# Kernel tuning notes

Hardware: AMD Instinct MI355X
Metric: run time of the kernel (lower is better)

The kernel has to match this reference:

```python
import jax, jax.numpy as jnp
import numpy as np

_SAMPLING_EPS = 1e-5
B, V = 256, 128000


def _apply_min_p(logits, min_p):
    # probs >= min_p * max_prob  <=>  keep; else logit -> -inf
    probs = jax.nn.softmax(logits, axis=-1)
    max_probs = jnp.max(probs, axis=-1, keepdims=True)
    keep = probs >= (min_p[:, None] * max_probs)
    return jnp.where(keep, logits, -jnp.inf)


def _apply_top_k_top_p(logits, top_k, top_p):
    # Sort ascending once; derive per-row keep-thresholds for both filters.
    logits_sort = jnp.sort(logits, axis=-1)  # [B, V] ascending
    # top-k threshold: value at position V-k (kth largest)
    k_idx = jnp.clip(V - top_k, 0, V - 1).astype(jnp.int32)
    k_thresh = jnp.take_along_axis(logits_sort, k_idx[:, None], axis=-1)  # [B,1]
    # top-p: on ascending-sorted probs, token is kept iff cumsum > 1 - p
    probs_sort = jax.nn.softmax(logits_sort, axis=-1)
    probs_cum = jnp.cumsum(probs_sort, axis=-1)
    kept = probs_cum > (1.0 - top_p[:, None])
    kept = kept.at[:, -1].set(True)  # always keep the max-prob token
    p_thresh = jnp.min(jnp.where(kept, logits_sort, jnp.inf), axis=-1, keepdims=True)
    thresh = jnp.maximum(k_thresh, p_thresh)
    return jnp.where(logits >= thresh, logits, -jnp.inf)


def setup_inputs() -> dict:
    key = jax.random.key(0)
    k1, k2, k3, k4, k5 = jax.random.split(key, 5)
    logits = jax.random.normal(k1, (B, V), jnp.float32)
    temperature = jax.random.uniform(k2, (B,), jnp.float32, 0.1, 1.5)
    temperature = temperature.at[:8].set(0.0)  # greedy rows
    min_p = jax.random.uniform(k3, (B,), jnp.float32, 0.0, 0.2)
    top_k = jax.random.randint(k4, (B,), 1, 64).astype(jnp.int32)
    top_p = jax.random.uniform(k5, (B,), jnp.float32, 0.5, 1.0)
    return {"logits": logits, "temperature": temperature, "min_p": min_p,
            "top_k": top_k, "top_p": top_p}


def reference(logits, temperature, min_p, top_k, top_p):
    logits = logits.astype(jnp.float32)
    greedy = jnp.argmax(logits, axis=-1)  # [B]
    # safe temperature divide (greedy rows have temp ~ 0 but are overridden)
    safe_t = jnp.where(temperature < _SAMPLING_EPS, 1.0, temperature)
    scaled = logits / safe_t[:, None]
    scaled = _apply_min_p(scaled, min_p)
    masked = _apply_top_k_top_p(scaled, top_k, top_p)
    # Gumbel-max trick == categorical sampling from softmax(masked)
    u = jax.random.uniform(jax.random.key(42), masked.shape, jnp.float32, 1e-10, 1.0)
    gumbel = -jnp.log(-jnp.log(u))
    random_sampled = jnp.argmax(masked + gumbel, axis=-1)
    sampled = jnp.where(temperature < _SAMPLING_EPS, greedy, random_sampled)
    return sampled[:, None]  # sampled_token_ids [B, 1]
```

## Files before the change

### kernel.cpp

```cpp
#include <hip/hip_runtime.h>
#include <stdint.h>

typedef unsigned long long u64;
typedef unsigned int u32;

#define VOCAB 128000
#define NV4   32000
#define NROWS 256
#define BLK   1024
#define NW    16
#define NB    4096
#define CAPL  4096
#define SEPS  1e-5f
#define LN2X40 27.725887222397812f

__device__ __forceinline__ u32 f2key(float f){
  u32 u = __float_as_uint(f);
  return (u & 0x80000000u) ? ~u : (u | 0x80000000u);
}
__device__ __forceinline__ float key2f(u32 k){
  u32 u = (k & 0x80000000u) ? (k ^ 0x80000000u) : ~k;
  return __uint_as_float(u);
}

__device__ __forceinline__ void tf2x32(u32 x0, u32 x1, u32 &o0, u32 &o1){
  const u32 k0 = 0u, k1 = 42u, k2 = 0u ^ 42u ^ 0x1BD11BDAu;
  x0 += k0; x1 += k1;
#define TFR(r) { x0 += x1; x1 = (x1 << (r)) | (x1 >> (32 - (r))); x1 ^= x0; }
  TFR(13) TFR(15) TFR(26) TFR(6)
  x0 += k1; x1 += k2 + 1u;
  TFR(17) TFR(29) TFR(16) TFR(24)
  x0 += k2; x1 += k0 + 2u;
  TFR(13) TFR(15) TFR(26) TFR(6)
  x0 += k0; x1 += k1 + 3u;
  TFR(17) TFR(29) TFR(16) TFR(24)
  x0 += k1; x1 += k2 + 4u;
  TFR(13) TFR(15) TFR(26) TFR(6)
  x0 += k2; x1 += k0 + 5u;
#undef TFR
  o0 = x0; o1 = x1;
}
__device__ __forceinline__ u32 gumbel_bits(u32 i){
  u32 o0, o1; tf2x32(0u, i, o0, o1);
  return o0 ^ o1;
}
__device__ __forceinline__ float bits2gumbel(u32 b){
  float f = __uint_as_float(0x3F800000u | (b >> 9)) - 1.0f;
  float u = fmaxf(1e-10f, f + 1e-10f);
  return -logf(-logf(u));
}

__device__ __forceinline__ void cross4096_u32(
    const u32* arr, u32* aux, u32 target, u32* out_idx, u32* out_before, int t)
{
  aux[t] = arr[4*t+0] + arr[4*t+1] + arr[4*t+2] + arr[4*t+3];
  __syncthreads();
  if (t < 64){
    u32 gs = 0u;
    #pragma unroll
    for (int j=0;j<16;j++) gs += aux[t*16+j];
    u32 pref = gs;
    #pragma unroll
    for (int d=1; d<64; d<<=1){ u32 v = __shfl_up(pref, d, 64); if (t >= d) pref += v; }
    u64 bal = __ballot(pref > target);
    int g = bal ? (__ffsll((long long)bal) - 1) : 63;
    u32 pg = __shfl(pref, g, 64);
    u32 gg = __shfl(gs, g, 64);
    if (t == 0){
      u32 c = pg - gg;
      u32 idx = (u32)(g*64 + 63);
      for (int j=0;j<16;j++){
        u32 v = aux[g*16+j];
        if (c + v > target){
          int base = (g*16+j)*4;
          for (int q=0;q<4;q++){
            u32 w = arr[base+q];
            if (c + w > target){ idx = (u32)(base+q); goto doneu; }
            c += w;
          }
        }
        c += v;
      }
      doneu:
      *out_idx = idx; *out_before = c;
    }
  }
}

__device__ __forceinline__ void cross4096_u64(
    const u64* arr, u64* aux, u64 target, u32* out_idx, u64* out_before, int t)
{
  aux[t] = arr[4*t+0] + arr[4*t+1] + arr[4*t+2] + arr[4*t+3];
  __syncthreads();
  if (t < 64){
    u64 gs = 0ull;
    #pragma unroll
    for (int j=0;j<16;j++) gs += aux[t*16+j];
    u64 pref = gs;
    #pragma unroll
    for (int d=1; d<64; d<<=1){
      u64 v = __shfl_up((unsigned long long)pref, d, 64); if (t >= d) pref += v;
    }
    u64 bal = __ballot(pref > target);
    int g = bal ? (__ffsll((long long)bal) - 1) : 63;
    u64 pg = __shfl((unsigned long long)pref, g, 64);
    u64 gg = __shfl((unsigned long long)gs, g, 64);
    if (t == 0){
      u64 c = pg - gg;
      u32 idx = (u32)(g*64 + 63);
      for (int j=0;j<16;j++){
        u64 v = aux[g*16+j];
        if (c + v > target){
          int base = (g*16+j)*4;
          for (int q=0;q<4;q++){
            u64 w = arr[base+q];
            if (c + w > target){ idx = (u32)(base+q); goto donev; }
            c += w;
          }
        }
        c += v;
      }
      donev:
      *out_idx = idx; *out_before = c;
    }
  }
}

__device__ __forceinline__ void cross4096_mass(
    const u64* arr, u64* aux, float topp_v, u64* out_target,
    u32* out_idx, u64* out_before, int t)
{
  aux[t] = arr[4*t+0] + arr[4*t+1] + arr[4*t+2] + arr[4*t+3];
  __syncthreads();
  if (t < 64){
    u64 gs = 0ull;
    #pragma unroll
    for (int j=0;j<16;j++) gs += aux[t*16+j];
    u64 pref = gs;
    #pragma unroll
    for (int d=1; d<64; d<<=1){
      u64 v = __shfl_up((unsigned long long)pref, d, 64); if (t >= d) pref += v;
    }
    u64 total = __shfl((unsigned long long)pref, 63, 64);
    u64 target = (u64)((double)(1.0f - topp_v) * (double)total);
    u64 bal = __ballot(pref > target);
    int g = bal ? (__ffsll((long long)bal) - 1) : 63;
    u64 pg = __shfl((unsigned long long)pref, g, 64);
    u64 gg = __shfl((unsigned long long)gs, g, 64);
    if (t == 0){
      u64 c = pg - gg;
      u32 idx = (u32)(g*64 + 63);
      for (int j=0;j<16;j++){
        u64 v = aux[g*16+j];
        if (c + v > target){
          int base = (g*16+j)*4;
          for (int q=0;q<4;q++){
            u64 w = arr[base+q];
            if (c + w > target){ idx = (u32)(base+q); goto donem; }
            c += w;
          }
        }
        c += v;
      }
      donem:
      *out_target = target; *out_idx = idx; *out_before = c;
    }
  }
}

__device__ __forceinline__ void cross256_u32(const u32* arr, u32 target, u32* out_idx, int t){
  if (t < 64){
    u32 gs = arr[4*t+0]+arr[4*t+1]+arr[4*t+2]+arr[4*t+3];
    u32 pref = gs;
    #pragma unroll
    for (int d=1; d<64; d<<=1){ u32 v=__shfl_up(pref,d,64); if (t>=d) pref+=v; }
    u64 bal = __ballot(pref > target);
    int g = bal ? (__ffsll((long long)bal)-1) : 63;
    u32 pg=__shfl(pref,g,64), gg=__shfl(gs,g,64);
    if (t==0){
      u32 c = pg-gg; u32 idx=(u32)(g*4+3);
      for (int q=0;q<4;q++){ u32 w=arr[g*4+q]; if (c+w>target){ idx=(u32)(g*4+q); break; } c+=w; }
      *out_idx = idx;
    }
  }
}
__device__ __forceinline__ void cross256_u64(const u64* arr, u64 target, u32* out_idx, int t){
  if (t < 64){
    u64 gs = arr[4*t+0]+arr[4*t+1]+arr[4*t+2]+arr[4*t+3];
    u64 pref = gs;
    #pragma unroll
    for (int d=1; d<64; d<<=1){
      u64 v=__shfl_up((unsigned long long)pref,d,64); if (t>=d) pref+=v;
    }
    u64 bal = __ballot(pref > target);
    int g = bal ? (__ffsll((long long)bal)-1) : 63;
    u64 pg=__shfl((unsigned long long)pref,g,64), gg=__shfl((unsigned long long)gs,g,64);
    if (t==0){
      u64 c = pg-gg; u32 idx=(u32)(g*4+3);
      for (int q=0;q<4;q++){ u64 w=arr[g*4+q]; if (c+w>target){ idx=(u32)(g*4+q); break; } c+=w; }
      *out_idx = idx;
    }
  }
}

__device__ __forceinline__ void msmerge(float &m1, float &S1, float m2, float S2){
  float mm = fmaxf(m1, m2);
  if (mm == -INFINITY){ m1 = mm; S1 = 0.0f; return; }
  S1 = S1*__expf(m1-mm) + S2*__expf(m2-mm);
  m1 = mm;
}

__device__ __forceinline__ void argmax_write(
    float best, u32 bi, float* wrf, u32* wru, int ln, int wv, int b, int* out)
{
  #pragma unroll
  for (int d=32; d>0; d>>=1){
    float c2=__shfl_down(best,d,64); u32 i2=__shfl_down(bi,d,64);
    if (c2>best || (c2==best && i2<bi)){best=c2;bi=i2;}
  }
  if (ln==0){ wrf[wv]=best; wru[wv]=bi; }
  __syncthreads();
  if (wv==0){
    float b1=(ln<NW)?wrf[ln]:-INFINITY; u32 i1=(ln<NW)?wru[ln]:0xFFFFFFFFu;
    #pragma unroll
    for (int d=32; d>0; d>>=1){
      float b2=__shfl_down(b1,d,64); u32 i2=__shfl_down(i1,d,64);
      if (b2>b1 || (b2==b1 && i2<i1)){b1=b2;i1=i2;}
    }
    if (ln==0) out[b]=(int)i1;
  }
}

__global__ __launch_bounds__(BLK) void k_all(
    const float* __restrict__ logits, const float* __restrict__ temp,
    const float* __restrict__ minp, const int* __restrict__ topk,
    const float* __restrict__ topp, int* __restrict__ out)
{
  __shared__ u32 cnt[NB];
  __shared__ u64 massI[2*NB];
  __shared__ u64 list[CAPL];
  __shared__ u64 aux64[BLK];
  __shared__ float wrf1[NW], wrf2[NW];
  __shared__ u32  wru1[NW], wru2[NW];
  __shared__ float sh_m, sh_Z;
  __shared__ u32 sh_lstar, sh_len, sh_idx, sh_bef32, sh_u1, sh_u2, sh_u3;
  __shared__ u64 sh_bef64, sh_tfix;

  u32* aux32 = (u32*)aux64;

  const int b = blockIdx.x;
  const int t = threadIdx.x;
  const int ln = t & 63, wv = t >> 6;
  const float T = temp[b];
  const float* row = logits + (size_t)b * VOCAB;
  const float4* row4 = (const float4*)row;

  if (T < SEPS){
    float M = -INFINITY; u32 Mi = 0xFFFFFFFFu;
    for (int i=t; i<NV4; i+=BLK){
      float4 q = row4[i];
      #pragma unroll
      for (int j=0;j<4;j++){
        float l = (&q.x)[j]; u32 gi = (u32)(i*4+j);
        if (l > M){ M = l; Mi = gi; }
      }
    }
    argmax_write(M, Mi, wrf1, wru1, ln, wv, b, out);
    return;
  }

  const float invT = 1.0f / T;
  for (int i=t;i<NB;i+=BLK) cnt[i]=0u;
  for (int i=t;i<2*NB;i+=BLK) massI[i]=0ull;
  if (t==0) sh_len=0u;
  __syncthreads();

  float ms0=-INFINITY,S0=0.0f, ms1=-INFINITY,S1=0.0f,
        ms2=-INFINITY,S2=0.0f, ms3=-INFINITY,S3=0.0f;
#define ONLINE(LV, MS, SS) { \
    float l_ = (LV); \
    atomicAdd(&cnt[f2key(l_)>>20], 1u); \
    float s_ = l_ * invT; \
    float d_ = s_ - MS; \
    float e_ = __expf(-fabsf(d_)); \
    if (d_ > 0.0f){ SS = fmaf(SS, e_, 1.0f); MS = s_; } else { SS += e_; } \
  }
  for (int i=t; i<NV4; i+=2*BLK){
    float4 qa = row4[i];
    int i2 = i + BLK; bool h2 = (i2 < NV4);
    float4 qb; if (h2) qb = row4[i2];
    ONLINE(qa.x,ms0,S0) ONLINE(qa.y,ms1,S1) ONLINE(qa.z,ms2,S2) ONLINE(qa.w,ms3,S3)
    if (h2){
      ONLINE(qb.x,ms0,S0) ONLINE(qb.y,ms1,S1) ONLINE(qb.z,ms2,S2) ONLINE(qb.w,ms3,S3)
    }
  }
#undef ONLINE
  msmerge(ms0,S0,ms1,S1); msmerge(ms2,S2,ms3,S3); msmerge(ms0,S0,ms2,S2);
  #pragma unroll
  for (int d=32; d>0; d>>=1){
    float mz = __shfl_down(ms0, d, 64); float Sz = __shfl_down(S0, d, 64);
    msmerge(ms0, S0, mz, Sz);
  }
  if (ln==0){ wrf1[wv]=ms0; wrf2[wv]=S0; }
  __syncthreads();
  if (wv==0){
    float m1 = (ln<NW)? wrf1[ln] : -INFINITY;
    float Sx = (ln<NW)? wrf2[ln] : 0.0f;
    #pragma unroll
    for (int d=32; d>0; d>>=1){
      float mz=__shfl_down(m1,d,64); float Sz=__shfl_down(Sx,d,64);
      msmerge(m1, Sx, mz, Sz);
    }
    if (ln==0){ sh_m = m1; sh_Z = Sx; }
  }
  __syncthreads();
  const float m = sh_m, Z = sh_Z;

  int tk = topk[b]; if (tk < 1) tk = 1; if (tk > VOCAB) tk = VOCAB;
  cross4096_u32(cnt, aux32, (u32)(VOCAB - tk), &sh_idx, &sh_bef32, t);
  __syncthreads();
  const u32 b1k = sh_idx;
  const u32 r1  = (u32)(VOCAB - tk + 1) - sh_bef32;

  if (wv==0){
    const float rhs = minp[b] * (1.0f / Z);
    u32 lo = 0u, hi = 0xFF800000u;
    while (hi - lo > 64u){
      u32 step = (hi - lo) >> 6;
      u32 k = lo + (u32)(ln + 1) * step;
      float e = __expf(fmaf(key2f(k), invT, -m));
      u64 bal = __ballot((e / Z) >= rhs);
      if (bal){
        u32 g = (u32)(__ffsll((long long)bal) - 1);
        hi = lo + (g + 1u) * step;
        lo = lo + g * step;
      } else {
        lo += 64u * step;
      }
    }
    u32 k = lo + 1u + (u32)ln;
    bool ok = (k <= hi);
    float e = __expf(fmaf(key2f(k), invT, -m));
    u64 bal = __ballot(ok && ((e / Z) >= rhs));
    if (ln==0) sh_lstar = bal ? (lo + 1u + (u32)(__ffsll((long long)bal) - 1)) : hi;
  }
  __syncthreads();
  const u32 lstar = sh_lstar;
  const u32 bl = lstar >> 20;

  {
    u32 pa=0u, pc=0u;
    for (int i=t;i<NB;i+=BLK){
      u32 c = cnt[i];
      if ((u32)i > bl)   pa += c;
      if ((u32)i >= b1k) pc += c;
    }
    #pragma unroll
    for (int d=32; d>0; d>>=1){ pa += __shfl_down(pa,d,64); pc += __shfl_down(pc,d,64); }
    if (ln==0){ wru1[wv]=pa; wru2[wv]=pc; }
    __syncthreads();
    if (t==0){
      u32 a=0u, c2=0u;
      for (int w=0; w<NW; w++){ a += wru1[w]; c2 += wru2[w]; }
      sh_u1 = a; sh_u2 = c2;
    }
    __syncthreads();
  }
  const u32 Kmin = sh_u1;
  const bool kcert = (Kmin >= (u32)tk);
  const u32 CLB = kcert ? b1k : bl;
  const u32 listlen = kcert ? sh_u2 : (Kmin + cnt[bl]);
  const bool fastOK = (listlen <= (u32)CAPL);
  const float cs = LN2X40 - m;

  u32 kc = 0u;
#define P2E(LV, IDX) { \
    float l_ = (LV); u32 key_ = f2key(l_); u32 bk_ = key_ >> 20; \
    if (key_ >= lstar){ \
      kc++; \
      u64 lm_ = (u64)__expf(fmaf(l_, invT, cs)); \
      if (lm_) atomicAdd(&massI[(bk_<<1) | (u32)(t&1)], lm_); \
    } \
    if (fastOK && bk_ >= CLB){ \
      u32 p_ = atomicAdd(&sh_len, 1u); \
      if (p_ < CAPL) list[p_] = ((u64)key_ << 32) | (u64)(u32)(IDX); \
    } \
  }
  for (int i=t; i<NV4; i+=2*BLK){
    float4 qa = row4[i];
    int i2 = i + BLK; bool h2 = (i2 < NV4);
    float4 qb; if (h2) qb = row4[i2];
    P2E(qa.x, i*4+0) P2E(qa.y, i*4+1) P2E(qa.z, i*4+2) P2E(qa.w, i*4+3)
    if (h2){
      P2E(qb.x, i2*4+0) P2E(qb.y, i2*4+1) P2E(qb.z, i2*4+2) P2E(qb.w, i2*4+3)
    }
  }
#undef P2E
  #pragma unroll
  for (int d=32; d>0; d>>=1) kc += __shfl_down(kc, d, 64);
  if (ln==0) wru1[wv] = kc;
  __syncthreads();
  if (t==0){ u32 K2=0u; for (int w=0;w<NW;w++) K2 += wru1[w]; sh_u3 = K2; }
  {
    u64 g0 = massI[8*t+0] + massI[8*t+1];
    u64 g1 = massI[8*t+2] + massI[8*t+3];
    u64 g2 = massI[8*t+4] + massI[8*t+5];
    u64 g3 = massI[8*t+6] + massI[8*t+7];
    __syncthreads();
    massI[4*t+0]=g0; massI[4*t+1]=g1; massI[4*t+2]=g2; massI[4*t+3]=g3;
  }
  __syncthreads();
  const u32 K = sh_u3;
  const bool kval = (K >= (u32)tk);
  const u32 llen = sh_len;

  cross4096_mass(massI, aux64, topp[b], &sh_tfix, &sh_idx, &sh_bef64, t);
  __syncthreads();
  const u32 b1p = sh_idx;
  const u64 t1  = sh_tfix - sh_bef64;
  const bool needK = kval && (b1p <= b1k);
  const bool needP = (!kval) || (b1p >= b1k);

  u32 kkey = 0u, pkey = 0u;

  if (fastOK){
    if (needK){
      for (int i=t;i<NB;i+=BLK) cnt[i]=0u;
      __syncthreads();
      for (u32 i=t; i<llen; i+=BLK){
        u32 key = (u32)(list[i]>>32);
        if ((key>>20) == b1k) atomicAdd(&cnt[(key>>8)&0xFFFu], 1u);
      }
      __syncthreads();
      cross4096_u32(cnt, aux32, r1-1u, &sh_idx, &sh_bef32, t);
      __syncthreads();
      u32 b2k = sh_idx, r2 = r1 - sh_bef32;
      u32 prefk = (b1k<<12) | b2k;
      for (int i=t;i<256;i+=BLK) cnt[i]=0u;
      __syncthreads();
      for (u32 i=t; i<llen; i+=BLK){
        u32 key = (u32)(list[i]>>32);
        if ((key>>8) == prefk) atomicAdd(&cnt[key&0xFFu], 1u);
      }
      __syncthreads();
      cross256_u32(cnt, r2-1u, &sh_idx, t);
      __syncthreads();
      kkey = (prefk<<8) | sh_idx;
    }
    if (needP){
      for (int i=t;i<NB;i+=BLK) massI[i]=0ull;
      __syncthreads();
      for (u32 i=t; i<llen; i+=BLK){
        u32 key = (u32)(list[i]>>32);
        if ((key>>20) == b1p && key >= lstar){
          u64 lm = (u64)__expf(fmaf(key2f(key), invT, cs));
          if (lm) atomicAdd(&massI[(key>>8)&0xFFFu], lm);
        }
      }
      __syncthreads();
      cross4096_u64(massI, aux64, t1, &sh_idx, &sh_bef64, t);
      __syncthreads();
      u32 b2p = sh_idx; u64 t2 = t1 - sh_bef64;
      u32 prefp = (b1p<<12) | b2p;
      for (int i=t;i<256;i+=BLK) massI[i]=0ull;
      __syncthreads();
      for (u32 i=t; i<llen; i+=BLK){
        u32 key = (u32)(list[i]>>32);
        if ((key>>8) == prefp && key >= lstar){
          u64 lm = (u64)__expf(fmaf(key2f(key), invT, cs));
          if (lm) atomicAdd(&massI[key&0xFFu], lm);
        }
      }
      __syncthreads();
      cross256_u64(massI, t2, &sh_idx, t);
      __syncthreads();
      pkey = (prefp<<8) | sh_idx;
    }
    const u32 thrkey = kkey > pkey ? kkey : pkey;

    float best = -INFINITY; u32 bi = 0xFFFFFFFFu;
    for (u32 i=t; i<llen; i+=BLK){
      u64 e = list[i];
      u32 key = (u32)(e>>32);
      if (key >= thrkey){
        u32 idx = (u32)e;
        u32 c = (u32)b * (u32)VOCAB + idx;
        float cand = key2f(key)*invT + bits2gumbel(gumbel_bits(c));
        if (cand > best || (cand == best && idx < bi)){ best = cand; bi = idx; }
      }
    }
    argmax_write(best, bi, wrf1, wru1, ln, wv, b, out);
    return;
  }

  for (int i=t;i<NB;i+=BLK){ cnt[i]=0u; massI[i]=0ull; }
  __syncthreads();
  for (int i=t; i<NV4; i+=BLK){
    float4 q = row4[i];
    #pragma unroll
    for (int j=0;j<4;j++){
      float l = (&q.x)[j]; u32 key = f2key(l); u32 hb = key>>20;
      if (needK && hb == b1k) atomicAdd(&cnt[(key>>8)&0xFFFu], 1u);
      if (needP && hb == b1p && key >= lstar){
        u64 lm = (u64)__expf(fmaf(l, invT, cs));
        if (lm) atomicAdd(&massI[(key>>8)&0xFFFu], lm);
      }
    }
  }
  __syncthreads();
  u32 b2k = 0u, r2 = 1u, b2p = 0u; u64 t2 = 0ull;
  if (needK){
    cross4096_u32(cnt, aux32, r1-1u, &sh_idx, &sh_bef32, t);
    __syncthreads();
    b2k = sh_idx; r2 = r1 - sh_bef32;
  }
  if (needP){
    cross4096_u64(massI, aux64, t1, &sh_idx, &sh_bef64, t);
    __syncthreads();
    b2p = sh_idx; t2 = t1 - sh_bef64;
  }
  const u32 prefk = (b1k<<12) | b2k;
  const u32 prefp = (b1p<<12) | b2p;
  for (int i=t;i<256;i+=BLK){ cnt[i]=0u; massI[i]=0ull; }
  __syncthreads();
  for (int i=t; i<NV4; i+=BLK){
    float4 q = row4[i];
    #pragma unroll
    for (int j=0;j<4;j++){
      float l = (&q.x)[j]; u32 key = f2key(l);
      if (needK && (key>>8) == prefk) atomicAdd(&cnt[key&0xFFu], 1u);
      if (needP && (key>>8) == prefp && key >= lstar){
        u64 lm = (u64)__expf(fmaf(l, invT, cs));
        if (lm) atomicAdd(&massI[key&0xFFu], lm);
      }
    }
  }
  __syncthreads();
  if (needK){
    cross256_u32(cnt, r2-1u, &sh_idx, t);
    __syncthreads();
    kkey = (prefk<<8) | sh_idx;
  }
  if (needP){
    cross256_u64(massI, t2, &sh_idx, t);
    __syncthreads();
    pkey = (prefp<<8) | sh_idx;
  }
  const float thrf = key2f(kkey > pkey ? kkey : pkey);
  float best = -INFINITY; u32 bi = 0xFFFFFFFFu;
  for (int i=t; i<NV4; i+=BLK){
    float4 q = row4[i];
    #pragma unroll
    for (int j=0;j<4;j++){
      float l = (&q.x)[j];
      if (l >= thrf){
        u32 idx = (u32)(i*4+j);
        u32 c = (u32)b * (u32)VOCAB + idx;
        float cand = l*invT + bits2gumbel(gumbel_bits(c));
        if (cand > best || (cand == best && idx < bi)){ best = cand; bi = idx; }
      }
    }
  }
  argmax_write(best, bi, wrf1, wru1, ln, wv, b, out);
}

extern "C" void kernel_launch(void* const* d_in, const int* in_sizes, int n_in,
                              void* d_out, int out_size, void* d_ws, size_t ws_size,
                              hipStream_t stream)
{
  const float* logits = (const float*)d_in[0];
  const float* temp   = (const float*)d_in[1];
  const float* minp   = (const float*)d_in[2];
  const int*   topk   = (const int*)d_in[3];
  const float* topp   = (const float*)d_in[4];
  int* out = (int*)d_out;

  hipLaunchKernelGGL(k_all, dim3(NROWS), dim3(BLK), 0, stream,
                     logits, temp, minp, topk, topp, out);
}
```

Before: 60.18 us.

## Fuse histogram, softmax mass and candidate collection into one speculative pass

A 2048-element sample of each row picks a speculative high-bucket cutoff. A single pass over the row then builds the count histogram, per-bucket exponential mass relative to the bucket edge, the running max key, and a ballot-compacted list of candidate tokens above the cutoff. This replaces the separate online-softmax pass and the second full pass. Z and the top-p bucket are derived in double precision from the per-bucket mass, and a fallback path re-scans the row when the speculation or list capacity fails. The change adds shared-memory pressure (larger list, double arrays) and code complexity, and misses in the speculation cost an extra pass.

```diff
diff --git a/kernel.cpp b/kernel.cpp
--- a/kernel.cpp
+++ b/kernel.cpp
@@ -1,5 +1,6 @@
 #include <hip/hip_runtime.h>
 #include <stdint.h>
+#include <math.h>
 
 typedef unsigned long long u64;
 typedef unsigned int u32;
@@ -10,9 +11,10 @@
 #define BLK   1024
 #define NW    16
 #define NB    4096
-#define CAPL  4096
+#define CAPL  6144
 #define SEPS  1e-5f
-#define LN2X40 27.725887222397812f
+#define LN2X38 26.339592865845667f
+#define INV238 3.637978807091713e-12
 
 __device__ __forceinline__ u32 f2key(float f){
   u32 u = __float_as_uint(f);
@@ -168,6 +170,54 @@
   }
 }
 
+__device__ __forceinline__ void cross4096_f64eff(
+    const double* arr, double* aux, u32 bl, double kappa, double target,
+    u32* out_idx, double* out_before, int t)
+{
+  double s4 = 0.0;
+  #pragma unroll
+  for (int q=0;q<4;q++){
+    u32 i = (u32)(4*t+q);
+    double v = (i > bl) ? arr[i] : ((i == bl) ? kappa : 0.0);
+    s4 += v;
+  }
+  aux[t] = s4;
+  __syncthreads();
+  if (t < 64){
+    double gs = 0.0;
+    #pragma unroll
+    for (int j=0;j<16;j++) gs += aux[t*16+j];
+    double pref = gs;
+    #pragma unroll
+    for (int d=1; d<64; d<<=1){
+      double v = __shfl_up(pref, d, 64); if (t >= d) pref += v;
+    }
+    u64 bal = __ballot(pref > target);
+    int g = bal ? (__ffsll((long long)bal) - 1) : 63;
+    double pg = __shfl(pref, g, 64);
+    double gg = __shfl(gs, g, 64);
+    if (t == 0){
+      double c = pg - gg;
+      u32 idx = (u32)(g*64 + 63);
+      for (int j=0;j<16;j++){
+        double v = aux[g*16+j];
+        if (c + v > target){
+          int base = (g*16+j)*4;
+          for (int q=0;q<4;q++){
+            u32 i = (u32)(base+q);
+            double w = (i > bl) ? arr[i] : ((i == bl) ? kappa : 0.0);
+            if (c + w > target){ idx = i; goto donef; }
+            c += w;
+          }
+        }
+        c += v;
+      }
+      donef:
+      *out_idx = idx; *out_before = c;
+    }
+  }
+}
+
 __device__ __forceinline__ void cross256_u32(const u32* arr, u32 target, u32* out_idx, int t){
   if (t < 64){
     u32 gs = arr[4*t+0]+arr[4*t+1]+arr[4*t+2]+arr[4*t+3];
@@ -203,13 +253,6 @@
   }
 }
 
-__device__ __forceinline__ void msmerge(float &m1, float &S1, float m2, float S2){
-  float mm = fmaxf(m1, m2);
-  if (mm == -INFINITY){ m1 = mm; S1 = 0.0f; return; }
-  S1 = S1*__expf(m1-mm) + S2*__expf(m2-mm);
-  m1 = mm;
-}
-
 __device__ __forceinline__ void argmax_write(
     float best, u32 bi, float* wrf, u32* wru, int ln, int wv, int b, int* out)
 {
@@ -231,22 +274,25 @@
   }
 }
 
-__global__ __launch_bounds__(BLK) void k_all(
+__global__ __launch_bounds__(BLK) void k_fused(
     const float* __restrict__ logits, const float* __restrict__ temp,
     const float* __restrict__ minp, const int* __restrict__ topk,
     const float* __restrict__ topp, int* __restrict__ out)
 {
   __shared__ u32 cnt[NB];
-  __shared__ u64 massI[2*NB];
+  __shared__ u64 mass[NB];
   __shared__ u64 list[CAPL];
   __shared__ u64 aux64[BLK];
-  __shared__ float wrf1[NW], wrf2[NW];
+  __shared__ float wrf1[NW];
   __shared__ u32  wru1[NW], wru2[NW];
-  __shared__ float sh_m, sh_Z;
-  __shared__ u32 sh_lstar, sh_len, sh_idx, sh_bef32, sh_u1, sh_u2, sh_u3;
-  __shared__ u64 sh_bef64, sh_tfix;
+  __shared__ u64  wrull[NW];
+  __shared__ u32 sh_idx, sh_bef32, sh_lstar, sh_len, sh_a, sh_b, sh_c;
+  __shared__ u64 sh_bef64, sh_tfix, sh_ku;
+  __shared__ double sh_dz, sh_dsup;
 
   u32* aux32 = (u32*)aux64;
+  double* auxd = (double*)aux64;
+  double* absd = (double*)mass;
 
   const int b = blockIdx.x;
   const int t = threadIdx.x;
@@ -268,53 +314,80 @@
     argmax_write(M, Mi, wrf1, wru1, ln, wv, b, out);
     return;
   }
-
   const float invT = 1.0f / T;
+
   for (int i=t;i<NB;i+=BLK) cnt[i]=0u;
-  for (int i=t;i<2*NB;i+=BLK) massI[i]=0ull;
   if (t==0) sh_len=0u;
   __syncthreads();
-
-  float ms0=-INFINITY,S0=0.0f, ms1=-INFINITY,S1=0.0f,
-        ms2=-INFINITY,S2=0.0f, ms3=-INFINITY,S3=0.0f;
-#define ONLINE(LV, MS, SS) { \
-    float l_ = (LV); \
-    atomicAdd(&cnt[f2key(l_)>>20], 1u); \
-    float s_ = l_ * invT; \
-    float d_ = s_ - MS; \
-    float e_ = __expf(-fabsf(d_)); \
-    if (d_ > 0.0f){ SS = fmaf(SS, e_, 1.0f); MS = s_; } else { SS += e_; } \
-  }
+  for (int s=t; s<2048; s+=BLK){
+    int c = s >> 6, j = s & 63;
+    float l = row[c*4000 + j];
+    atomicAdd(&cnt[f2key(l)>>20], 1u);
+  }
+  __syncthreads();
+  cross4096_u32(cnt, aux32, 2016u, &sh_idx, &sh_bef32, t);
+  __syncthreads();
+  const u32 bspec = sh_idx;
+  const u32 keyspec = bspec << 20;
+  __syncthreads();
+  for (int i=t;i<NB;i+=BLK){ cnt[i]=0u; mass[i]=0ull; }
+  __syncthreads();
+
+  u32 km = 0u;
+#define P1E(LV, IDX) { \
+    float l_ = (LV); u32 key_ = f2key(l_); u32 bk_ = key_ >> 20; \
+    if (key_ > km) km = key_; \
+    atomicAdd(&cnt[bk_], 1u); \
+    float edge_ = key2f(bk_ << 20); \
+    atomicAdd(&mass[bk_], (u64)__expf(fmaf(l_ - edge_, invT, LN2X38))); \
+    bool cand_ = (key_ >= keyspec); \
+    u64 bal_ = __ballot(cand_); \
+    if (cand_){ \
+      u32 lead_ = (u32)__ffsll((long long)bal_) - 1u; \
+      u32 base_ = 0u; \
+      if ((u32)ln == lead_) base_ = atomicAdd(&sh_len, (u32)__popcll(bal_)); \
+      base_ = __shfl(base_, (int)lead_, 64); \
+      u32 p_ = base_ + (u32)__popcll(bal_ & ((1ull << ln) - 1ull)); \
+      if (p_ < CAPL) list[p_] = ((u64)key_ << 32) | (u64)(u32)(IDX); \
+    } }
   for (int i=t; i<NV4; i+=2*BLK){
     float4 qa = row4[i];
     int i2 = i + BLK; bool h2 = (i2 < NV4);
     float4 qb; if (h2) qb = row4[i2];
-    ONLINE(qa.x,ms0,S0) ONLINE(qa.y,ms1,S1) ONLINE(qa.z,ms2,S2) ONLINE(qa.w,ms3,S3)
+    P1E(qa.x, i*4+0) P1E(qa.y, i*4+1) P1E(qa.z, i*4+2) P1E(qa.w, i*4+3)
     if (h2){
-      ONLINE(qb.x,ms0,S0) ONLINE(qb.y,ms1,S1) ONLINE(qb.z,ms2,S2) ONLINE(qb.w,ms3,S3)
-    }
-  }
-#undef ONLINE
-  msmerge(ms0,S0,ms1,S1); msmerge(ms2,S2,ms3,S3); msmerge(ms0,S0,ms2,S2);
+      P1E(qb.x, i2*4+0) P1E(qb.y, i2*4+1) P1E(qb.z, i2*4+2) P1E(qb.w, i2*4+3)
+    }
+  }
+#undef P1E
   #pragma unroll
-  for (int d=32; d>0; d>>=1){
-    float mz = __shfl_down(ms0, d, 64); float Sz = __shfl_down(S0, d, 64);
-    msmerge(ms0, S0, mz, Sz);
-  }
-  if (ln==0){ wrf1[wv]=ms0; wrf2[wv]=S0; }
-  __syncthreads();
-  if (wv==0){
-    float m1 = (ln<NW)? wrf1[ln] : -INFINITY;
-    float Sx = (ln<NW)? wrf2[ln] : 0.0f;
-    #pragma unroll
-    for (int d=32; d>0; d>>=1){
-      float mz=__shfl_down(m1,d,64); float Sz=__shfl_down(Sx,d,64);
-      msmerge(m1, Sx, mz, Sz);
-    }
-    if (ln==0){ sh_m = m1; sh_Z = Sx; }
-  }
-  __syncthreads();
-  const float m = sh_m, Z = sh_Z;
+  for (int d=32; d>0; d>>=1){ u32 k2 = __shfl_down(km, d, 64); if (k2 > km) km = k2; }
+  if (ln==0) wru1[wv] = km;
+  __syncthreads();
+  if (t==0){
+    u32 kt = wru1[0];
+    for (int w=1; w<NW; w++) if (wru1[w] > kt) kt = wru1[w];
+    sh_a = kt;
+  }
+  __syncthreads();
+  const float m = key2f(sh_a) * invT;
+  const double invTd = (double)invT, md = (double)m;
+  const float csg = LN2X38 - m;
+
+  #pragma unroll
+  for (int q=0;q<4;q++){
+    int i0 = 4*t + q;
+    u64 lm = mass[i0];
+    absd[i0] = lm ? (double)lm * exp((double)key2f((u32)i0 << 20) * invTd - md) * INV238 : 0.0;
+  }
+  {
+    double s4 = absd[4*t]+absd[4*t+1]+absd[4*t+2]+absd[4*t+3];
+    auxd[t] = s4; __syncthreads();
+    for (int off=512; off>0; off>>=1){ if (t<off) auxd[t] += auxd[t+off]; __syncthreads(); }
+    if (t==0) sh_dz = auxd[0];
+    __syncthreads();
+  }
+  const float Z = (float)sh_dz;
 
   int tk = topk[b]; if (tk < 1) tk = 1; if (tk > VOCAB) tk = VOCAB;
   cross4096_u32(cnt, aux32, (u32)(VOCAB - tk), &sh_idx, &sh_bef32, t);
@@ -362,68 +435,92 @@
     if (t==0){
       u32 a=0u, c2=0u;
       for (int w=0; w<NW; w++){ a += wru1[w]; c2 += wru2[w]; }
-      sh_u1 = a; sh_u2 = c2;
-    }
-    __syncthreads();
-  }
-  const u32 Kmin = sh_u1;
+      sh_a = a; sh_b = c2;
+    }
+    __syncthreads();
+  }
+  const u32 Kmin = sh_a;
+  const u32 pc   = sh_b;
   const bool kcert = (Kmin >= (u32)tk);
   const u32 CLB = kcert ? b1k : bl;
-  const u32 listlen = kcert ? sh_u2 : (Kmin + cnt[bl]);
-  const bool fastOK = (listlen <= (u32)CAPL);
-  const float cs = LN2X40 - m;
-
-  u32 kc = 0u;
-#define P2E(LV, IDX) { \
-    float l_ = (LV); u32 key_ = f2key(l_); u32 bk_ = key_ >> 20; \
-    if (key_ >= lstar){ \
-      kc++; \
-      u64 lm_ = (u64)__expf(fmaf(l_, invT, cs)); \
-      if (lm_) atomicAdd(&massI[(bk_<<1) | (u32)(t&1)], lm_); \
-    } \
-    if (fastOK && bk_ >= CLB){ \
-      u32 p_ = atomicAdd(&sh_len, 1u); \
-      if (p_ < CAPL) list[p_] = ((u64)key_ << 32) | (u64)(u32)(IDX); \
-    } \
-  }
-  for (int i=t; i<NV4; i+=2*BLK){
-    float4 qa = row4[i];
-    int i2 = i + BLK; bool h2 = (i2 < NV4);
-    float4 qb; if (h2) qb = row4[i2];
-    P2E(qa.x, i*4+0) P2E(qa.y, i*4+1) P2E(qa.z, i*4+2) P2E(qa.w, i*4+3)
-    if (h2){
-      P2E(qb.x, i2*4+0) P2E(qb.y, i2*4+1) P2E(qb.z, i2*4+2) P2E(qb.w, i2*4+3)
-    }
-  }
-#undef P2E
-  #pragma unroll
-  for (int d=32; d>0; d>>=1) kc += __shfl_down(kc, d, 64);
-  if (ln==0) wru1[wv] = kc;
-  __syncthreads();
-  if (t==0){ u32 K2=0u; for (int w=0;w<NW;w++) K2 += wru1[w]; sh_u3 = K2; }
+
   {
-    u64 g0 = massI[8*t+0] + massI[8*t+1];
-    u64 g1 = massI[8*t+2] + massI[8*t+3];
-    u64 g2 = massI[8*t+4] + massI[8*t+5];
-    u64 g3 = massI[8*t+6] + massI[8*t+7];
-    __syncthreads();
-    massI[4*t+0]=g0; massI[4*t+1]=g1; massI[4*t+2]=g2; massI[4*t+3]=g3;
-  }
-  __syncthreads();
-  const u32 K = sh_u3;
-  const bool kval = (K >= (u32)tk);
-  const u32 llen = sh_len;
-
-  cross4096_mass(massI, aux64, topp[b], &sh_tfix, &sh_idx, &sh_bef64, t);
-  __syncthreads();
-  const u32 b1p = sh_idx;
-  const u64 t1  = sh_tfix - sh_bef64;
-  const bool needK = kval && (b1p <= b1k);
-  const bool needP = (!kval) || (b1p >= b1k);
+    double s4 = 0.0;
+    #pragma unroll
+    for (int q=0;q<4;q++){ u32 i=(u32)(4*t+q); if (i > bl) s4 += absd[i]; }
+    auxd[t] = s4; __syncthreads();
+    for (int off=512; off>0; off>>=1){ if (t<off) auxd[t] += auxd[t+off]; __syncthreads(); }
+    if (t==0) sh_dsup = auxd[0];
+    __syncthreads();
+  }
+  const double Msup = sh_dsup;
+  const double abl  = absd[bl];
+
+  const bool lok = (sh_len <= (u32)CAPL);
+  const u32 llen = lok ? sh_len : (u32)CAPL;
+  const bool blcov = (bl >= bspec);
+  bool fb = !lok;
+
+  bool kval = kcert;
+  double kappa = 0.0;
+  bool needK = false, needP = false;
+  u32 b1p = 0; double t1d = 0.0;
+
+  if (!fb && blcov){
+    u32 kcbl = 0; u64 ku = 0ull;
+    for (u32 i=t; i<llen; i+=BLK){
+      u64 e = list[i]; u32 key = (u32)(e>>32);
+      if ((key>>20) == bl && key >= lstar){
+        kcbl++;
+        ku += (u64)__expf(fmaf(key2f(key), invT, csg));
+      }
+    }
+    #pragma unroll
+    for (int d=32; d>0; d>>=1){
+      kcbl += __shfl_down(kcbl, d, 64);
+      ku   += __shfl_down((unsigned long long)ku, d, 64);
+    }
+    if (ln==0){ wru1[wv]=kcbl; wrull[wv]=ku; }
+    __syncthreads();
+    if (t==0){
+      u32 a=0u; u64 k2=0ull;
+      for (int w=0; w<NW; w++){ a += wru1[w]; k2 += wrull[w]; }
+      sh_c = a; sh_ku = k2;
+    }
+    __syncthreads();
+    kval = kcert || (Kmin + sh_c >= (u32)tk);
+    kappa = (double)sh_ku * INV238;
+
+    double target = (double)(1.0f - topp[b]) * (Msup + kappa);
+    cross4096_f64eff(absd, auxd, bl, kappa, target, &sh_idx, (double*)&aux64[BLK-2], t);
+    __syncthreads();
+    b1p = sh_idx;
+    t1d = target - *(double*)&aux64[BLK-2];
+    needK = kval && (b1p <= b1k);
+    needP = (!kval) || (b1p >= b1k);
+    if (needP && b1p < bspec) fb = true;
+    if (needK && b1k < bspec) fb = true;
+  } else if (!fb){
+    if (!kcert) fb = true;
+    else {
+      const float pv = topp[b];
+      double tgt0 = (double)(1.0f - pv) * Msup;
+      cross4096_f64eff(absd, auxd, bl, 0.0, tgt0, &sh_idx, (double*)&aux64[BLK-2], t);
+      __syncthreads();
+      u32 p0 = sh_idx;
+      __syncthreads();
+      double tgt1 = (double)(1.0f - pv) * (Msup + abl);
+      cross4096_f64eff(absd, auxd, bl, abl, tgt1, &sh_idx, (double*)&aux64[BLK-2], t);
+      __syncthreads();
+      u32 p1 = sh_idx;
+      if (p0 < b1k && p1 < b1k && b1k >= bspec){ needK = true; needP = false; kval = true; }
+      else fb = true;
+    }
+  }
 
   u32 kkey = 0u, pkey = 0u;
 
-  if (fastOK){
+  if (!fb){
     if (needK){
       for (int i=t;i<NB;i+=BLK) cnt[i]=0u;
       __syncthreads();
@@ -448,31 +545,32 @@
       kkey = (prefk<<8) | sh_idx;
     }
     if (needP){
-      for (int i=t;i<NB;i+=BLK) massI[i]=0ull;
-      __syncthreads();
+      for (int i=t;i<NB;i+=BLK) mass[i]=0ull;
+      __syncthreads();
+      const float edgep = key2f(b1p << 20);
       for (u32 i=t; i<llen; i+=BLK){
         u32 key = (u32)(list[i]>>32);
-        if ((key>>20) == b1p && key >= lstar){
-          u64 lm = (u64)__expf(fmaf(key2f(key), invT, cs));
-          if (lm) atomicAdd(&massI[(key>>8)&0xFFFu], lm);
-        }
-      }
-      __syncthreads();
-      cross4096_u64(massI, aux64, t1, &sh_idx, &sh_bef64, t);
-      __syncthreads();
-      u32 b2p = sh_idx; u64 t2 = t1 - sh_bef64;
+        if ((key>>20) == b1p && key >= lstar)
+          atomicAdd(&mass[(key>>8)&0xFFFu],
+                    (u64)__expf(fmaf(key2f(key) - edgep, invT, LN2X38)));
+      }
+      __syncthreads();
+      double scp = exp((double)edgep * invTd - md) * INV238;
+      u64 t1u = (u64)(t1d / scp);
+      cross4096_u64(mass, aux64, t1u, &sh_idx, &sh_bef64, t);
+      __syncthreads();
+      u32 b2p = sh_idx; u64 t2 = t1u - sh_bef64;
       u32 prefp = (b1p<<12) | b2p;
-      for (int i=t;i<256;i+=BLK) massI[i]=0ull;
+      for (int i=t;i<256;i+=BLK) mass[i]=0ull;
       __syncthreads();
       for (u32 i=t; i<llen; i+=BLK){
         u32 key = (u32)(list[i]>>32);
-        if ((key>>8) == prefp && key >= lstar){
-          u64 lm = (u64)__expf(fmaf(key2f(key), invT, cs));
-          if (lm) atomicAdd(&massI[key&0xFFu], lm);
-        }
-      }
-      __syncthreads();
-      cross256_u64(massI, t2, &sh_idx, t);
+        if ((key>>8) == prefp && key >= lstar)
+          atomicAdd(&mass[key&0xFFu],
+                    (u64)__expf(fmaf(key2f(key) - edgep, invT, LN2X38)));
+      }
+      __syncthreads();
+      cross256_u64(mass, t2, &sh_idx, t);
       __syncthreads();
       pkey = (prefp<<8) | sh_idx;
     }
@@ -493,56 +591,176 @@
     return;
   }
 
-  for (int i=t;i<NB;i+=BLK){ cnt[i]=0u; massI[i]=0ull; }
+  const bool fblok = ((kcert ? pc : (Kmin + cnt[bl])) <= (u32)CAPL);
+  for (int i=t;i<NB;i+=BLK) mass[i]=0ull;
+  if (t==0) sh_len=0u;
+  __syncthreads();
+  u32 kc = 0u;
+#define P2E(LV, IDX) { \
+    float l_ = (LV); u32 key_ = f2key(l_); \
+    if (key_ >= lstar){ \
+      kc++; \
+      u64 lm_ = (u64)__expf(fmaf(l_, invT, csg)); \
+      if (lm_) atomicAdd(&mass[key_>>20], lm_); \
+    } \
+    bool cand_ = fblok && ((key_>>20) >= CLB); \
+    u64 bal_ = __ballot(cand_); \
+    if (cand_){ \
+      u32 lead_ = (u32)__ffsll((long long)bal_) - 1u; \
+      u32 base_ = 0u; \
+      if ((u32)ln == lead_) base_ = atomicAdd(&sh_len, (u32)__popcll(bal_)); \
+      base_ = __shfl(base_, (int)lead_, 64); \
+      u32 p_ = base_ + (u32)__popcll(bal_ & ((1ull << ln) - 1ull)); \
+      if (p_ < CAPL) list[p_] = ((u64)key_ << 32) | (u64)(u32)(IDX); \
+    } }
+  for (int i=t; i<NV4; i+=2*BLK){
+    float4 qa = row4[i];
+    int i2 = i + BLK; bool h2 = (i2 < NV4);
+    float4 qb; if (h2) qb = row4[i2];
+    P2E(qa.x, i*4+0) P2E(qa.y, i*4+1) P2E(qa.z, i*4+2) P2E(qa.w, i*4+3)
+    if (h2){
+      P2E(qb.x, i2*4+0) P2E(qb.y, i2*4+1) P2E(qb.z, i2*4+2) P2E(qb.w, i2*4+3)
+    }
+  }
+#undef P2E
+  #pragma unroll
+  for (int d=32; d>0; d>>=1) kc += __shfl_down(kc, d, 64);
+  if (ln==0) wru1[wv] = kc;
+  __syncthreads();
+  if (t==0){ u32 K2=0u; for (int w=0;w<NW;w++) K2 += wru1[w]; sh_c = K2; }
+  __syncthreads();
+  const u32 K = sh_c;
+  const bool fkval = (K >= (u32)tk);
+  const u32 fllen = (sh_len <= (u32)CAPL) ? sh_len : (u32)CAPL;
+
+  cross4096_mass(mass, aux64, topp[b], &sh_tfix, &sh_idx, &sh_bef64, t);
+  __syncthreads();
+  const u32 fb1p = sh_idx;
+  const u64 ft1  = sh_tfix - sh_bef64;
+  const bool fneedK = fkval && (fb1p <= b1k);
+  const bool fneedP = (!fkval) || (fb1p >= b1k);
+
+  kkey = 0u; pkey = 0u;
+
+  if (fblok){
+    if (fneedK){
+      for (int i=t;i<NB;i+=BLK) cnt[i]=0u;
+      __syncthreads();
+      for (u32 i=t; i<fllen; i+=BLK){
+        u32 key = (u32)(list[i]>>32);
+        if ((key>>20) == b1k) atomicAdd(&cnt[(key>>8)&0xFFFu], 1u);
+      }
+      __syncthreads();
+      cross4096_u32(cnt, aux32, r1-1u, &sh_idx, &sh_bef32, t);
+      __syncthreads();
+      u32 b2k = sh_idx, r2 = r1 - sh_bef32;
+      u32 prefk = (b1k<<12) | b2k;
+      for (int i=t;i<256;i+=BLK) cnt[i]=0u;
+      __syncthreads();
+      for (u32 i=t; i<fllen; i+=BLK){
+        u32 key = (u32)(list[i]>>32);
+        if ((key>>8) == prefk) atomicAdd(&cnt[key&0xFFu], 1u);
+      }
+      __syncthreads();
+      cross256_u32(cnt, r2-1u, &sh_idx, t);
+      __syncthreads();
+      kkey = (prefk<<8) | sh_idx;
+    }
+    if (fneedP){
+      for (int i=t;i<NB;i+=BLK) mass[i]=0ull;
+      __syncthreads();
+      for (u32 i=t; i<fllen; i+=BLK){
+        u32 key = (u32)(list[i]>>32);
+        if ((key>>20) == fb1p && key >= lstar){
+          u64 lm = (u64)__expf(fmaf(key2f(key), invT, csg));
+          if (lm) atomicAdd(&mass[(key>>8)&0xFFFu], lm);
+        }
+      }
+      __syncthreads();
+      cross4096_u64(mass, aux64, ft1, &sh_idx, &sh_bef64, t);
+      __syncthreads();
+      u32 b2p = sh_idx; u64 t2 = ft1 - sh_bef64;
+      u32 prefp = (fb1p<<12) | b2p;
+      for (int i=t;i<256;i+=BLK) mass[i]=0ull;
+      __syncthreads();
+      for (u32 i=t; i<fllen; i+=BLK){
+        u32 key = (u32)(list[i]>>32);
+        if ((key>>8) == prefp && key >= lstar){
+          u64 lm = (u64)__expf(fmaf(key2f(key), invT, csg));
+          if (lm) atomicAdd(&mass[key&0xFFu], lm);
+        }
+      }
+      __syncthreads();
+      cross256_u64(mass, t2, &sh_idx, t);
+      __syncthreads();
+      pkey = (prefp<<8) | sh_idx;
+    }
+    const u32 thrkey = kkey > pkey ? kkey : pkey;
+    float best = -INFINITY; u32 bi = 0xFFFFFFFFu;
+    for (u32 i=t; i<fllen; i+=BLK){
+      u64 e = list[i];
+      u32 key = (u32)(e>>32);
+      if (key >= thrkey){
+        u32 idx = (u32)e;
+        u32 c = (u32)b * (u32)VOCAB + idx;
+        float cand = key2f(key)*invT + bits2gumbel(gumbel_bits(c));
+        if (cand > best || (cand == best && idx < bi)){ best = cand; bi = idx; }
+      }
+    }
+    argmax_write(best, bi, wrf1, wru1, ln, wv, b, out);
+    return;
+  }
+
+  for (int i=t;i<NB;i+=BLK){ cnt[i]=0u; mass[i]=0ull; }
   __syncthreads();
   for (int i=t; i<NV4; i+=BLK){
     float4 q = row4[i];
     #pragma unroll
     for (int j=0;j<4;j++){
       float l = (&q.x)[j]; u32 key = f2key(l); u32 hb = key>>20;
-      if (needK && hb == b1k) atomicAdd(&cnt[(key>>8)&0xFFFu], 1u);
-      if (needP && hb == b1p && key >= lstar){
-        u64 lm = (u64)__expf(fmaf(l, invT, cs));
-        if (lm) atomicAdd(&massI[(key>>8)&0xFFFu], lm);
+      if (fneedK && hb == b1k) atomicAdd(&cnt[(key>>8)&0xFFFu], 1u);
+      if (fneedP && hb == fb1p && key >= lstar){
+        u64 lm = (u64)__expf(fmaf(l, invT, csg));
+        if (lm) atomicAdd(&mass[(key>>8)&0xFFFu], lm);
       }
     }
   }
   __syncthreads();
   u32 b2k = 0u, r2 = 1u, b2p = 0u; u64 t2 = 0ull;
-  if (needK){
+  if (fneedK){
     cross4096_u32(cnt, aux32, r1-1u, &sh_idx, &sh_bef32, t);
     __syncthreads();
     b2k = sh_idx; r2 = r1 - sh_bef32;
   }
-  if (needP){
-    cross4096_u64(massI, aux64, t1, &sh_idx, &sh_bef64, t);
-    __syncthreads();
-    b2p = sh_idx; t2 = t1 - sh_bef64;
+  if (fneedP){
+    cross4096_u64(mass, aux64, ft1, &sh_idx, &sh_bef64, t);
+    __syncthreads();
+    b2p = sh_idx; t2 = ft1 - sh_bef64;
   }
   const u32 prefk = (b1k<<12) | b2k;
-  const u32 prefp = (b1p<<12) | b2p;
-  for (int i=t;i<256;i+=BLK){ cnt[i]=0u; massI[i]=0ull; }
+  const u32 prefp = (fb1p<<12) | b2p;
+  for (int i=t;i<256;i+=BLK){ cnt[i]=0u; mass[i]=0ull; }
   __syncthreads();
   for (int i=t; i<NV4; i+=BLK){
     float4 q = row4[i];
     #pragma unroll
     for (int j=0;j<4;j++){
       float l = (&q.x)[j]; u32 key = f2key(l);
-      if (needK && (key>>8) == prefk) atomicAdd(&cnt[key&0xFFu], 1u);
-      if (needP && (key>>8) == prefp && key >= lstar){
-        u64 lm = (u64)__expf(fmaf(l, invT, cs));
-        if (lm) atomicAdd(&massI[key&0xFFu], lm);
-      }
-    }
-  }
-  __syncthreads();
-  if (needK){
+      if (fneedK && (key>>8) == prefk) atomicAdd(&cnt[key&0xFFu], 1u);
+      if (fneedP && (key>>8) == prefp && key >= lstar){
+        u64 lm = (u64)__expf(fmaf(l, invT, csg));
+        if (lm) atomicAdd(&mass[key&0xFFu], lm);
+      }
+    }
+  }
+  __syncthreads();
+  if (fneedK){
     cross256_u32(cnt, r2-1u, &sh_idx, t);
     __syncthreads();
     kkey = (prefk<<8) | sh_idx;
   }
-  if (needP){
-    cross256_u64(massI, t2, &sh_idx, t);
+  if (fneedP){
+    cross256_u64(mass, t2, &sh_idx, t);
     __syncthreads();
     pkey = (prefp<<8) | sh_idx;
   }
@@ -575,6 +793,6 @@
   const float* topp   = (const float*)d_in[4];
   int* out = (int*)d_out;
 
-  hipLaunchKernelGGL(k_all, dim3(NROWS), dim3(BLK), 0, stream,
+  hipLaunchKernelGGL(k_fused, dim3(NROWS), dim3(BLK), 0, stream,
                      logits, temp, minp, topk, topp, out);
 }
```

New measurement: 68.34 us. 13.6% more time.

## Shrink shared memory footprint and simplify softmax pass to raise occupancy

Applied to the files above, without the earlier changes.

The online max/sum softmax merge in the first pass is replaced by a key-max plus plain exp-sum, rescaled afterwards. The double-banked mass histogram is collapsed to a single bank and the candidate list capacity is halved. Together these cut LDS use from roughly 112KB to about 72KB, which may allow two blocks per CU, and remove per-element rescaling work. The risks are more atomic contention on the single-bank mass histogram, overflow of exp(l/T) without max subtraction for small temperatures, and more rows falling off the fast path because of the smaller list capacity.

```diff
diff --git a/kernel.cpp b/kernel.cpp
--- a/kernel.cpp
+++ b/kernel.cpp
@@ -10,7 +10,7 @@
 #define BLK   1024
 #define NW    16
 #define NB    4096
-#define CAPL  4096
+#define CAPL  2048
 #define SEPS  1e-5f
 #define LN2X40 27.725887222397812f
 
@@ -203,13 +203,6 @@
   }
 }
 
-__device__ __forceinline__ void msmerge(float &m1, float &S1, float m2, float S2){
-  float mm = fmaxf(m1, m2);
-  if (mm == -INFINITY){ m1 = mm; S1 = 0.0f; return; }
-  S1 = S1*__expf(m1-mm) + S2*__expf(m2-mm);
-  m1 = mm;
-}
-
 __device__ __forceinline__ void argmax_write(
     float best, u32 bi, float* wrf, u32* wru, int ln, int wv, int b, int* out)
 {
@@ -237,13 +230,13 @@
     const float* __restrict__ topp, int* __restrict__ out)
 {
   __shared__ u32 cnt[NB];
-  __shared__ u64 massI[2*NB];
+  __shared__ u64 massI[NB];
   __shared__ u64 list[CAPL];
   __shared__ u64 aux64[BLK];
-  __shared__ float wrf1[NW], wrf2[NW];
+  __shared__ float wrf1[NW];
   __shared__ u32  wru1[NW], wru2[NW];
-  __shared__ float sh_m, sh_Z;
-  __shared__ u32 sh_lstar, sh_len, sh_idx, sh_bef32, sh_u1, sh_u2, sh_u3;
+  __shared__ u32 sh_kmax, sh_lstar, sh_len, sh_idx, sh_bef32, sh_u1, sh_u2, sh_u3;
+  __shared__ float sh_Z;
   __shared__ u64 sh_bef64, sh_tfix;
 
   u32* aux32 = (u32*)aux64;
@@ -270,51 +263,42 @@
   }
 
   const float invT = 1.0f / T;
-  for (int i=t;i<NB;i+=BLK) cnt[i]=0u;
-  for (int i=t;i<2*NB;i+=BLK) massI[i]=0ull;
+  for (int i=t;i<NB;i+=BLK){ cnt[i]=0u; massI[i]=0ull; }
   if (t==0) sh_len=0u;
   __syncthreads();
 
-  float ms0=-INFINITY,S0=0.0f, ms1=-INFINITY,S1=0.0f,
-        ms2=-INFINITY,S2=0.0f, ms3=-INFINITY,S3=0.0f;
-#define ONLINE(LV, MS, SS) { \
-    float l_ = (LV); \
-    atomicAdd(&cnt[f2key(l_)>>20], 1u); \
-    float s_ = l_ * invT; \
-    float d_ = s_ - MS; \
-    float e_ = __expf(-fabsf(d_)); \
-    if (d_ > 0.0f){ SS = fmaf(SS, e_, 1.0f); MS = s_; } else { SS += e_; } \
-  }
+  u32 km = 0u;
+  float S0=0.0f,S1=0.0f,S2=0.0f,S3=0.0f;
+#define P1E(LV, SS) { \
+    float l_ = (LV); u32 k_ = f2key(l_); \
+    if (k_ > km) km = k_; \
+    atomicAdd(&cnt[k_>>20], 1u); \
+    SS += __expf(l_ * invT); }
   for (int i=t; i<NV4; i+=2*BLK){
     float4 qa = row4[i];
     int i2 = i + BLK; bool h2 = (i2 < NV4);
     float4 qb; if (h2) qb = row4[i2];
-    ONLINE(qa.x,ms0,S0) ONLINE(qa.y,ms1,S1) ONLINE(qa.z,ms2,S2) ONLINE(qa.w,ms3,S3)
-    if (h2){
-      ONLINE(qb.x,ms0,S0) ONLINE(qb.y,ms1,S1) ONLINE(qb.z,ms2,S2) ONLINE(qb.w,ms3,S3)
-    }
-  }
-#undef ONLINE
-  msmerge(ms0,S0,ms1,S1); msmerge(ms2,S2,ms3,S3); msmerge(ms0,S0,ms2,S2);
+    P1E(qa.x,S0) P1E(qa.y,S1) P1E(qa.z,S2) P1E(qa.w,S3)
+    if (h2){ P1E(qb.x,S0) P1E(qb.y,S1) P1E(qb.z,S2) P1E(qb.w,S3) }
+  }
+#undef P1E
+  float S = (S0+S1)+(S2+S3);
   #pragma unroll
   for (int d=32; d>0; d>>=1){
-    float mz = __shfl_down(ms0, d, 64); float Sz = __shfl_down(S0, d, 64);
-    msmerge(ms0, S0, mz, Sz);
-  }
-  if (ln==0){ wrf1[wv]=ms0; wrf2[wv]=S0; }
-  __syncthreads();
-  if (wv==0){
-    float m1 = (ln<NW)? wrf1[ln] : -INFINITY;
-    float Sx = (ln<NW)? wrf2[ln] : 0.0f;
-    #pragma unroll
-    for (int d=32; d>0; d>>=1){
-      float mz=__shfl_down(m1,d,64); float Sz=__shfl_down(Sx,d,64);
-      msmerge(m1, Sx, mz, Sz);
-    }
-    if (ln==0){ sh_m = m1; sh_Z = Sx; }
-  }
-  __syncthreads();
-  const float m = sh_m, Z = sh_Z;
+    S += __shfl_down(S, d, 64);
+    u32 k2 = __shfl_down(km, d, 64); if (k2 > km) km = k2;
+  }
+  if (ln==0){ wrf1[wv]=S; wru1[wv]=km; }
+  __syncthreads();
+  if (t==0){
+    float St=0.0f; u32 kt=0u;
+    for (int w=0; w<NW; w++){ St += wrf1[w]; if (wru1[w]>kt) kt=wru1[w]; }
+    sh_kmax = kt;
+    sh_Z = St;
+  }
+  __syncthreads();
+  const float m = key2f(sh_kmax) * invT;
+  const float Z = sh_Z * __expf(-m);
 
   int tk = topk[b]; if (tk < 1) tk = 1; if (tk > VOCAB) tk = VOCAB;
   cross4096_u32(cnt, aux32, (u32)(VOCAB - tk), &sh_idx, &sh_bef32, t);
@@ -375,13 +359,13 @@
 
   u32 kc = 0u;
 #define P2E(LV, IDX) { \
-    float l_ = (LV); u32 key_ = f2key(l_); u32 bk_ = key_ >> 20; \
+    float l_ = (LV); u32 key_ = f2key(l_); \
     if (key_ >= lstar){ \
       kc++; \
       u64 lm_ = (u64)__expf(fmaf(l_, invT, cs)); \
-      if (lm_) atomicAdd(&massI[(bk_<<1) | (u32)(t&1)], lm_); \
+      if (lm_) atomicAdd(&massI[key_>>20], lm_); \
     } \
-    if (fastOK && bk_ >= CLB){ \
+    if (fastOK && (key_>>20) >= CLB){ \
       u32 p_ = atomicAdd(&sh_len, 1u); \
       if (p_ < CAPL) list[p_] = ((u64)key_ << 32) | (u64)(u32)(IDX); \
     } \
@@ -401,18 +385,10 @@
   if (ln==0) wru1[wv] = kc;
   __syncthreads();
   if (t==0){ u32 K2=0u; for (int w=0;w<NW;w++) K2 += wru1[w]; sh_u3 = K2; }
-  {
-    u64 g0 = massI[8*t+0] + massI[8*t+1];
-    u64 g1 = massI[8*t+2] + massI[8*t+3];
-    u64 g2 = massI[8*t+4] + massI[8*t+5];
-    u64 g3 = massI[8*t+6] + massI[8*t+7];
-    __syncthreads();
-    massI[4*t+0]=g0; massI[4*t+1]=g1; massI[4*t+2]=g2; massI[4*t+3]=g3;
-  }
   __syncthreads();
   const u32 K = sh_u3;
   const bool kval = (K >= (u32)tk);
-  const u32 llen = sh_len;
+  const u32 llen = (sh_len <= (u32)CAPL) ? sh_len : (u32)CAPL;
 
   cross4096_mass(massI, aux64, topp[b], &sh_tfix, &sh_idx, &sh_bef64, t);
   __syncthreads();
```

New measurement: 57.36 us (median of 2 runs). -4.7%, faster.
